# Kernel optimization log

Measured on AMD Instinct MI355X. Metric: run time of the kernel, lower is better.

The kernel has to match this reference:

```python
import jax, jax.numpy as jnp
import numpy as np

NEG_SLOPE = 0.2
EPS = 1e-5

N_NODES = 50000
N_GRAPHS = 500
NODES_PER_GRAPH = 100
N_EDGES = 500000
F_IN = 16
F_GRAPH = 4
HID = 64
N_CLASSES = 2


def setup_inputs() -> dict:
    key = jax.random.key(0)
    ks = jax.random.split(key, 32)
    x = jax.random.normal(ks[0], (N_NODES, F_IN), dtype=jnp.float32)
    # intra-graph random edges: dst lives in the same 100-node block as src
    src = jax.random.randint(ks[1], (N_EDGES,), 0, N_NODES)
    dst = (src // NODES_PER_GRAPH) * NODES_PER_GRAPH + jax.random.randint(ks[2], (N_EDGES,), 0, NODES_PER_GRAPH)
    edge_index = jnp.stack([src, dst]).astype(jnp.int64)
    graph_input = jax.random.normal(ks[3], (N_GRAPHS, F_GRAPH), dtype=jnp.float32)
    batch = (jnp.arange(N_NODES) // NODES_PER_GRAPH).astype(jnp.int64)

    def w(k, shape, scale=0.1):
        return (jax.random.normal(k, shape, dtype=jnp.float32) * scale)

    inp = dict(x=x, edge_index=edge_index, graph_input=graph_input, batch=batch)
    # GraphNorm params
    inp['gn_w'] = jnp.ones((F_IN,), jnp.float32)
    inp['gn_b'] = w(ks[4], (F_IN,))
    inp['gn_ms'] = jnp.ones((F_IN,), jnp.float32)
    inp['W1'] = w(ks[5], (F_IN, 4 * HID))
    inp['as1'] = w(ks[6], (4, HID)); inp['ad1'] = w(ks[7], (4, HID))
    inp['b1'] = w(ks[8], (4 * HID,))
    inp['W2'] = w(ks[9], (4 * HID, 4 * HID))
    inp['as2'] = w(ks[10], (4, HID)); inp['ad2'] = w(ks[11], (4, HID))
    inp['b2'] = w(ks[12], (4 * HID,))
    inp['W3'] = w(ks[13], (4 * HID, HID))
    inp['as3'] = w(ks[14], (1, HID)); inp['ad3'] = w(ks[15], (1, HID))
    inp['b3'] = w(ks[16], (HID,))
    # BatchNorm1d (eval mode) over [HID + F_GRAPH]
    D = HID + F_GRAPH
    inp['bn_g'] = 1.0 + w(ks[17], (D,))
    inp['bn_b'] = w(ks[18], (D,))
    inp['bn_m'] = jnp.zeros((D,), jnp.float32)
    inp['bn_v'] = jnp.ones((D,), jnp.float32)
    # Dense head
    inp['Wd1'] = w(ks[19], (D, HID)); inp['bd1'] = w(ks[20], (HID,))
    inp['Wd2'] = w(ks[21], (HID, HID)); inp['bd2'] = w(ks[22], (HID,))
    inp['Wo'] = w(ks[23], (HID, N_CLASSES)); inp['bo'] = w(ks[24], (N_CLASSES,))
    return inp


def _segment_softmax(e, seg, n):
    m = jax.ops.segment_max(e, seg, num_segments=n)
    ex = jnp.exp(e - m[seg])
    s = jax.ops.segment_sum(ex, seg, num_segments=n)
    return ex / s[seg]


def _gat_conv(x, src, dst, W, att_src, att_dst, b):
    N = x.shape[0]
    H, C = att_src.shape
    loop = jnp.arange(N)
    src = jnp.concatenate([src, loop])  # PyG GATConv adds self-loops
    dst = jnp.concatenate([dst, loop])
    h = (x @ W).reshape(N, H, C)
    a_src = (h * att_src).sum(-1)  # [N,H]
    a_dst = (h * att_dst).sum(-1)
    e = jax.nn.leaky_relu(a_src[src] + a_dst[dst], NEG_SLOPE)  # [E,H]
    alpha = _segment_softmax(e, dst, N)
    out = jax.ops.segment_sum(h[src] * alpha[:, :, None], dst, num_segments=N)
    return out.reshape(N, H * C) + b


def _graph_norm(x, batch, n_graphs, w, b, ms):
    cnt = jax.ops.segment_sum(jnp.ones((x.shape[0],), x.dtype), batch, num_segments=n_graphs)[:, None]
    mean = jax.ops.segment_sum(x, batch, num_segments=n_graphs) / cnt
    out = x - mean[batch] * ms
    var = jax.ops.segment_sum(out * out, batch, num_segments=n_graphs) / cnt
    return w * out / jnp.sqrt(var[batch] + EPS) + b


def _global_mean_pool(x, batch, n_graphs):
    cnt = jax.ops.segment_sum(jnp.ones((x.shape[0],), x.dtype), batch, num_segments=n_graphs)[:, None]
    return jax.ops.segment_sum(x, batch, num_segments=n_graphs) / cnt


def reference(x, edge_index, graph_input, batch,
              gn_w, gn_b, gn_ms,
              W1, as1, ad1, b1,
              W2, as2, ad2, b2,
              W3, as3, ad3, b3,
              bn_g, bn_b, bn_m, bn_v,
              Wd1, bd1, Wd2, bd2, Wo, bo):
    src, dst = edge_index[0], edge_index[1]
    G = graph_input.shape[0]
    h = _graph_norm(x, batch, G, gn_w, gn_b, gn_ms)
    # dropout is a no-op in eval
    h = jax.nn.elu(_gat_conv(h, src, dst, W1, as1, ad1, b1))
    h = jax.nn.elu(_gat_conv(h, src, dst, W2, as2, ad2, b2))
    h = _gat_conv(h, src, dst, W3, as3, ad3, b3)
    g = _global_mean_pool(h, batch, G)
    g = jnp.concatenate([g, graph_input], axis=1)
    g = (g - bn_m) / jnp.sqrt(bn_v + EPS) * bn_g + bn_b  # BatchNorm1d eval
    g = jax.nn.selu(g @ Wd1 + bd1)
    g = jax.nn.selu(g @ Wd2 + bd2)
    g = g @ Wo + bo
    return jax.nn.softmax(g, axis=1)
```

## Files before the change

kernel.cpp:

```cpp
#include <hip/hip_runtime.h>
#include <math.h>

#define N_NODES 50000
#define N_ROWS_PAD 50048
#define N_GRAPHS 500
#define NPG 100
#define N_EDGES 500000
#define F_IN 16
#define HID 64
#define EW_CAP 1408

#define SELU_SCALE 1.0507009873554804934193349852946f
#define SELU_ALPHA 1.6732632423543772848170429916717f

typedef __attribute__((ext_vector_type(8))) short short8;
typedef __attribute__((ext_vector_type(8))) unsigned short ushort8;
typedef __attribute__((ext_vector_type(4))) float floatx4;

__device__ __forceinline__ float lrelu(float x){ return x > 0.f ? x : 0.2f * x; }
__device__ __forceinline__ float eluf(float x){ return x > 0.f ? x : expf(x) - 1.f; }
__device__ __forceinline__ float seluf(float x){
    return x > 0.f ? SELU_SCALE * x : SELU_SCALE * (SELU_ALPHA * (expf(x) - 1.f));
}
__device__ __forceinline__ unsigned short f2bf(float x){
    unsigned u = __float_as_uint(x);
    return (unsigned short)((u + 0x7FFFu + ((u >> 16) & 1u)) >> 16);
}
__device__ __forceinline__ float bf2f(unsigned short u){
    return __uint_as_float((unsigned)u << 16);
}
__device__ __forceinline__ float bf2f_lo(unsigned u){
    return __uint_as_float(u << 16);
}
__device__ __forceinline__ float bf2f_hi(unsigned u){
    return __uint_as_float(u & 0xFFFF0000u);
}

__global__ void k_count(const int* __restrict__ dst, int* __restrict__ counts){
    int e = blockIdx.x * 256 + threadIdx.x;
    if (e < N_EDGES) atomicAdd(&counts[dst[e]], 1);
}

__global__ void k_local_scan(const int* __restrict__ counts, int* __restrict__ local_off,
                             int* __restrict__ graph_tot){
    __shared__ int s[128];
    int g = blockIdx.x, t = threadIdx.x;
    int v = (t < NPG) ? counts[g * NPG + t] : 0;
    s[t] = v; __syncthreads();
    for (int o = 1; o < 128; o <<= 1){
        int x = (t >= o) ? s[t - o] : 0;
        __syncthreads();
        s[t] += x;
        __syncthreads();
    }
    if (t < NPG) local_off[g * NPG + t] = s[t] - v;
    if (t == 127) graph_tot[g] = s[127];
}

__global__ void k_graph_scan(const int* __restrict__ graph_tot, int* __restrict__ graph_base){
    __shared__ int s[512];
    int t = threadIdx.x;
    int v = (t < N_GRAPHS) ? graph_tot[t] : 0;
    s[t] = v; __syncthreads();
    for (int o = 1; o < 512; o <<= 1){
        int x = (t >= o) ? s[t - o] : 0;
        __syncthreads();
        s[t] += x;
        __syncthreads();
    }
    if (t < N_GRAPHS) graph_base[t] = s[t] - v;
}

__global__ void k_off(const int* __restrict__ local_off, const int* __restrict__ graph_base,
                      int* __restrict__ node_off, int* __restrict__ write_ptr){
    int n = blockIdx.x * 256 + threadIdx.x;
    if (n < N_NODES){
        int v = local_off[n] + graph_base[n / NPG];
        node_off[n] = v;
        write_ptr[n] = v;
    }
}

__global__ void k_scatter(const int* __restrict__ src, const int* __restrict__ dst,
                          int* __restrict__ write_ptr, int* __restrict__ csr){
    int e = blockIdx.x * 256 + threadIdx.x;
    if (e < N_EDGES){
        int d = dst[e];
        int pos = atomicAdd(&write_ptr[d], 1);
        int b = (d / NPG) * NPG;
        csr[pos] = (src[e] - b) | ((d - b) << 8);
    }
}

__global__ void k_prep(const float* __restrict__ W1, const float* __restrict__ as1,
                       const float* __restrict__ ad1,
                       const float* __restrict__ W2, const float* __restrict__ as2,
                       const float* __restrict__ ad2,
                       const float* __restrict__ W3, const float* __restrict__ as3,
                       const float* __restrict__ ad3,
                       unsigned short* __restrict__ Wp2, unsigned short* __restrict__ Wp3,
                       float* __restrict__ M1f,
                       unsigned short* __restrict__ Mp2, unsigned short* __restrict__ Mp3){
    int id = blockIdx.x * 256 + threadIdx.x;
    if (id < 65536){
        int k = id >> 8, n = id & 255;
        Wp2[(((k >> 3) * 256) + n) * 8 + (k & 7)] = f2bf(W2[id]);
    } else if (id < 81920){
        int i = id - 65536;
        int k = i >> 6, n = i & 63;
        Wp3[(((k >> 3) * 64) + n) * 8 + (k & 7)] = f2bf(W3[i]);
    } else if (id < 82048){
        int i = id - 81920;
        int k = i >> 3, j = i & 7;
        int h = j & 3;
        const float* a = (j < 4) ? as1 : ad1;
        float s = 0.f;
        for (int c = 0; c < 64; c++) s += W1[k * 256 + h * 64 + c] * a[h * 64 + c];
        M1f[k * 8 + j] = s;
    } else if (id < 86144){
        int i = id - 82048;
        int k = i >> 4, col = i & 15;
        float s = 0.f;
        if (col < 8){
            int h = col & 3;
            const float* a = (col < 4) ? as2 : ad2;
            for (int c = 0; c < 64; c++) s += W2[k * 256 + h * 64 + c] * a[h * 64 + c];
        }
        Mp2[((k >> 3) * 16 + col) * 8 + (k & 7)] = f2bf(s);
    } else if (id < 90240){
        int i = id - 86144;
        int k = i >> 4, col = i & 15;
        float s = 0.f;
        if (col < 2){
            const float* a = (col == 0) ? as3 : ad3;
            for (int c = 0; c < 64; c++) s += W3[k * 64 + c] * a[c];
        }
        Mp3[((k >> 3) * 16 + col) * 8 + (k & 7)] = f2bf(s);
    }
}

__global__ void k_gnorm(const float* __restrict__ x, const float* __restrict__ w,
                        const float* __restrict__ b, const float* __restrict__ ms,
                        const float* __restrict__ M1f,
                        float* __restrict__ y, float* __restrict__ lg1){
    __shared__ float sx[NPG * F_IN];
    __shared__ float red[16][16];
    __shared__ float meanS[16], varS[16];
    int g = blockIdx.x, t = threadIdx.x;
    for (int idx = t; idx < NPG * F_IN; idx += 256) sx[idx] = x[g * NPG * F_IN + idx];
    __syncthreads();
    int f = t & 15, grp = t >> 4;
    float p = 0.f;
    for (int i = grp; i < NPG; i += 16) p += sx[i * 16 + f];
    red[grp][f] = p; __syncthreads();
    if (t < 16){
        float s = 0.f;
        for (int i = 0; i < 16; i++) s += red[i][t];
        meanS[t] = s * (1.f / 100.f);
    }
    __syncthreads();
    float mm = meanS[f] * ms[f];
    p = 0.f;
    for (int i = grp; i < NPG; i += 16){ float v = sx[i * 16 + f] - mm; p += v * v; }
    red[grp][f] = p; __syncthreads();
    if (t < 16){
        float s = 0.f;
        for (int i = 0; i < 16; i++) s += red[i][t];
        varS[t] = s * (1.f / 100.f);
    }
    __syncthreads();
    for (int idx = t; idx < NPG * F_IN; idx += 256){
        int ff = idx & 15;
        float v = w[ff] * (sx[idx] - meanS[ff] * ms[ff]) * rsqrtf(varS[ff] + 1e-5f) + b[ff];
        sx[idx] = v;
        y[g * NPG * F_IN + idx] = v;
    }
    __syncthreads();
    for (int i = t; i < NPG * 8; i += 256){
        int n = i >> 3, j = i & 7;
        float s = 0.f;
        #pragma unroll
        for (int ff = 0; ff < 16; ff++) s += sx[n * 16 + ff] * M1f[ff * 8 + j];
        lg1[(size_t)(g * NPG + n) * 8 + j] = s;
    }
}

__global__ void __launch_bounds__(256)
k_gemm_tiled(const float* __restrict__ X, const float* __restrict__ W,
             unsigned short* __restrict__ Ybf, int N){
    __shared__ float As[64][17];
    __shared__ float Bs[16][256];
    int t = threadIdx.x;
    int r0 = blockIdx.x * 64;
    {
        int row = t >> 2, kq = t & 3;
        float4 v = (r0 + row < N) ? *(const float4*)&X[(size_t)(r0 + row) * 16 + kq * 4]
                                  : make_float4(0.f, 0.f, 0.f, 0.f);
        As[row][kq * 4 + 0] = v.x; As[row][kq * 4 + 1] = v.y;
        As[row][kq * 4 + 2] = v.z; As[row][kq * 4 + 3] = v.w;
    }
    for (int i = t; i < 1024; i += 256)
        *(float4*)&Bs[0][i * 4] = *(const float4*)&W[i * 4];
    __syncthreads();

    int c4 = t & 15, rsub = t >> 4;
    float acc[4][16];
    #pragma unroll
    for (int i = 0; i < 4; i++)
        #pragma unroll
        for (int j = 0; j < 16; j++) acc[i][j] = 0.f;

    for (int k = 0; k < 16; k++){
        float a_[4];
        #pragma unroll
        for (int i = 0; i < 4; i++) a_[i] = As[rsub + 16 * i][k];
        float4 b0 = *(const float4*)&Bs[k][c4 * 4];
        float4 b1 = *(const float4*)&Bs[k][64 + c4 * 4];
        float4 b2 = *(const float4*)&Bs[k][128 + c4 * 4];
        float4 b3 = *(const float4*)&Bs[k][192 + c4 * 4];
        float bv[16] = {b0.x, b0.y, b0.z, b0.w, b1.x, b1.y, b1.z, b1.w,
                        b2.x, b2.y, b2.z, b2.w, b3.x, b3.y, b3.z, b3.w};
        #pragma unroll
        for (int i = 0; i < 4; i++)
            #pragma unroll
            for (int j = 0; j < 16; j++) acc[i][j] = fmaf(a_[i], bv[j], acc[i][j]);
    }
    #pragma unroll
    for (int i = 0; i < 4; i++){
        int row = r0 + rsub + 16 * i;
        if (row < N){
            ushort8 ua, ub;
            #pragma unroll
            for (int m = 0; m < 8; m++){
                ua[m] = f2bf(acc[i][(m & 3) * 4 + (m >> 2)]);
                ub[m] = f2bf(acc[i][(m & 3) * 4 + 2 + (m >> 2)]);
            }
            *(ushort8*)&Ybf[(size_t)row * 256 + c4 * 16]     = ua;
            *(ushort8*)&Ybf[(size_t)row * 256 + c4 * 16 + 8] = ub;
        }
    }
}

template<int COLB, int LG>
__global__ void __launch_bounds__(256)
k_gemm_mfma(const unsigned short* __restrict__ Xb,
            const unsigned short* __restrict__ Wp,
            const unsigned short* __restrict__ Mp,
            unsigned short* __restrict__ Ybf, float* __restrict__ lg,
            int N, int K, int OUT){
    int b = blockIdx.x;
    if (COLB == 4){
        int xcd = b & 7, idx = b >> 3;
        b = xcd * (int)(gridDim.x >> 3) + idx;
    }
    int cb = b & (COLB - 1);
    int rb = b / COLB;

    int t = threadIdx.x;
    int wave = t >> 6, lane = t & 63;
    int quad = lane >> 4, ln = lane & 15;
    int r0 = rb * 64 + wave * 16;
    int c0 = cb * 64;

    floatx4 acc[4];
    #pragma unroll
    for (int f = 0; f < 4; f++) acc[f] = (floatx4){0.f, 0.f, 0.f, 0.f};
    floatx4 accL = (floatx4){0.f, 0.f, 0.f, 0.f};

    const unsigned short* aptr = Xb + (size_t)(r0 + ln) * K + quad * 8;
    for (int kt = 0; kt < K; kt += 32){
        short8 a = *(const short8*)(aptr + kt);
        int kc = (kt >> 3) + quad;
        #pragma unroll
        for (int f = 0; f < 4; f++){
            short8 bfr = *(const short8*)(Wp + ((size_t)kc * OUT + c0 + f * 16 + ln) * 8);
            acc[f] = __builtin_amdgcn_mfma_f32_16x16x32_bf16(a, bfr, acc[f], 0, 0, 0);
        }
        if (LG > 0){
            if (cb == 0){
                short8 m = *(const short8*)(Mp + ((size_t)kc * 16 + ln) * 8);
                accL = __builtin_amdgcn_mfma_f32_16x16x32_bf16(a, m, accL, 0, 0, 0);
            }
        }
    }
    int rowb = r0 + quad * 4;
    #pragma unroll
    for (int f = 0; f < 4; f++){
        int col = c0 + f * 16 + ln;
        #pragma unroll
        for (int rg = 0; rg < 4; rg++){
            int row = rowb + rg;
            if (row < N) Ybf[(size_t)row * OUT + col] = f2bf(acc[f][rg]);
        }
    }
    if (LG > 0){
        if (cb == 0 && ln < LG){
            #pragma unroll
            for (int rg = 0; rg < 4; rg++){
                int row = rowb + rg;
                if (row < N) lg[(size_t)row * LG + ln] = accL[rg];
            }
        }
    }
}

template<int ILVIN>
__global__ void __launch_bounds__(512)
k_fused4(const unsigned short* __restrict__ hbf, const float* __restrict__ lg,
         const float* __restrict__ bias,
         const int* __restrict__ csr, const int* __restrict__ noff,
         const int* __restrict__ cnt, unsigned short* __restrict__ out_bf){
    __shared__ __align__(16) unsigned short hl[ILVIN ? 16 : NPG * 256];
    __shared__ __align__(16) unsigned int edl[EW_CAP][4];
    __shared__ __align__(16) float asrcl[NPG * 4], adstl[NPG * 4];
    __shared__ __align__(16) float wselfl[NPG * 4], rsuml[NPG * 4];
    __shared__ int offl[NPG], cntl[NPG];

    int g = blockIdx.x, t = threadIdx.x;
    int wave = t >> 6, lane = t & 63;
    int base = g * NPG;

    int ebeg = noff[base];
    int etot = noff[base + NPG - 1] + cnt[base + NPG - 1] - ebeg;
    int eln = etot < EW_CAP ? etot : EW_CAP;

    if (!ILVIN){
        for (int i = t; i < NPG * 16; i += 512){
            int node = i >> 4, c4 = i & 15;
            const unsigned short* hr = hbf + (size_t)(base + node) * 256 + c4 * 4;
            ushort4 f0 = *(const ushort4*)(hr);
            ushort4 f1 = *(const ushort4*)(hr + 64);
            ushort4 f2 = *(const ushort4*)(hr + 128);
            ushort4 f3 = *(const ushort4*)(hr + 192);
            ushort8 lo, hi;
            lo[0] = f0.x; lo[1] = f1.x; lo[2] = f2.x; lo[3] = f3.x;
            lo[4] = f0.y; lo[5] = f1.y; lo[6] = f2.y; lo[7] = f3.y;
            hi[0] = f0.z; hi[1] = f1.z; hi[2] = f2.z; hi[3] = f3.z;
            hi[4] = f0.w; hi[5] = f1.w; hi[6] = f2.w; hi[7] = f3.w;
            *(ushort8*)&hl[node * 256 + c4 * 16]     = lo;
            *(ushort8*)&hl[node * 256 + c4 * 16 + 8] = hi;
        }
    }
    for (int i = t; i < eln; i += 512) edl[i][2] = (unsigned)csr[ebeg + i];
    if (t < NPG){
        offl[t] = noff[base + t];
        cntl[t] = cnt[base + t];
        const float* lp = lg + (size_t)(base + t) * 8;
        *(float4*)&asrcl[t * 4] = *(const float4*)lp;
        *(float4*)&adstl[t * 4] = *(const float4*)(lp + 4);
    }
    __syncthreads();

    for (int i = t; i < eln; i += 512){
        unsigned sd = edl[i][2];
        int s = sd & 0xFF, d = sd >> 8;
        float4 av = *(const float4*)&asrcl[s * 4];
        float4 dv = *(const float4*)&adstl[d * 4];
        unsigned w0 = f2bf(expf(lrelu(av.x + dv.x)));
        unsigned w1 = f2bf(expf(lrelu(av.y + dv.y)));
        unsigned w2 = f2bf(expf(lrelu(av.z + dv.z)));
        unsigned w3 = f2bf(expf(lrelu(av.w + dv.w)));
        edl[i][0] = w0 | (w1 << 16);
        edl[i][1] = w2 | (w3 << 16);
    }
    __syncthreads();

    if (t < NPG){
        int d = t;
        float4 av = *(const float4*)&asrcl[d * 4];
        float4 dv = *(const float4*)&adstl[d * 4];
        float ws0 = expf(lrelu(av.x + dv.x));
        float ws1 = expf(lrelu(av.y + dv.y));
        float ws2 = expf(lrelu(av.z + dv.z));
        float ws3 = expf(lrelu(av.w + dv.w));
        float s0 = ws0, s1 = ws1, s2 = ws2, s3 = ws3;
        int ebg = offl[d] - ebeg, n = cntl[d];
        for (int j = 0; j < n; j++){
            uint2 v = *(const uint2*)&edl[ebg + j][0];
            s0 += bf2f_lo(v.x); s1 += bf2f_hi(v.x);
            s2 += bf2f_lo(v.y); s3 += bf2f_hi(v.y);
        }
        *(float4*)&wselfl[d * 4] = make_float4(ws0, ws1, ws2, ws3);
        *(float4*)&rsuml[d * 4]  = make_float4(1.f / s0, 1.f / s1, 1.f / s2, 1.f / s3);
    }
    __syncthreads();

    float b0 = bias[lane], b1 = bias[64 + lane], b2 = bias[128 + lane], b3 = bias[192 + lane];
    for (int d = wave; d < NPG; d += 8){
        float4 ws = *(const float4*)&wselfl[d * 4];
        float4 rs = *(const float4*)&rsuml[d * 4];
        ushort4 hv = ILVIN ? *(const ushort4*)&hbf[(size_t)(base + d) * 256 + lane * 4]
                           : *(const ushort4*)&hl[d * 256 + lane * 4];
        float a0 = ws.x * bf2f(hv.x);
        float a1 = ws.y * bf2f(hv.y);
        float a2 = ws.z * bf2f(hv.z);
        float a3 = ws.w * bf2f(hv.w);
        int ebg = offl[d] - ebeg, n = cntl[d];
        int j = 0;
        #pragma unroll 1
        for (; j + 4 <= n; j += 4){
            #pragma unroll
            for (int k = 0; k < 4; k++){
                uint4 v = *(const uint4*)&edl[ebg + j + k][0];
                int s = (int)(v.z & 0xFFu);
                ushort4 x = ILVIN ? *(const ushort4*)&hbf[(size_t)(base + s) * 256 + lane * 4]
                                  : *(const ushort4*)&hl[s * 256 + lane * 4];
                a0 = fmaf(bf2f_lo(v.x), bf2f(x.x), a0);
                a1 = fmaf(bf2f_hi(v.x), bf2f(x.y), a1);
                a2 = fmaf(bf2f_lo(v.y), bf2f(x.z), a2);
                a3 = fmaf(bf2f_hi(v.y), bf2f(x.w), a3);
            }
        }
        for (; j < n; j++){
            uint4 v = *(const uint4*)&edl[ebg + j][0];
            int s = (int)(v.z & 0xFFu);
            ushort4 x = ILVIN ? *(const ushort4*)&hbf[(size_t)(base + s) * 256 + lane * 4]
                              : *(const ushort4*)&hl[s * 256 + lane * 4];
            a0 = fmaf(bf2f_lo(v.x), bf2f(x.x), a0);
            a1 = fmaf(bf2f_hi(v.x), bf2f(x.y), a1);
            a2 = fmaf(bf2f_lo(v.y), bf2f(x.z), a2);
            a3 = fmaf(bf2f_hi(v.y), bf2f(x.w), a3);
        }
        size_t ob = (size_t)(base + d) * 256 + lane;
        out_bf[ob]       = f2bf(eluf(a0 * rs.x + b0));
        out_bf[ob + 64]  = f2bf(eluf(a1 * rs.y + b1));
        out_bf[ob + 128] = f2bf(eluf(a2 * rs.z + b2));
        out_bf[ob + 192] = f2bf(eluf(a3 * rs.w + b3));
    }
}

__global__ void __launch_bounds__(512)
k_fused1(const unsigned short* __restrict__ hbf, const float* __restrict__ lg3,
         const float* __restrict__ bias,
         const int* __restrict__ csr, const int* __restrict__ noff,
         const int* __restrict__ cnt, float* __restrict__ out){
    __shared__ __align__(16) unsigned int edl[EW_CAP][2];
    __shared__ float asrcl[NPG], adstl[NPG];
    __shared__ float wselfl[NPG], rsuml[NPG];
    __shared__ int offl[NPG], cntl[NPG];

    int g = blockIdx.x, t = threadIdx.x;
    int wave = t >> 6, lane = t & 63;
    int base = g * NPG;

    int ebeg = noff[base];
    int etot = noff[base + NPG - 1] + cnt[base + NPG - 1] - ebeg;
    int eln = etot < EW_CAP ? etot : EW_CAP;

    for (int i = t; i < eln; i += 512) edl[i][1] = (unsigned)csr[ebeg + i];
    if (t < NPG){
        offl[t] = noff[base + t];
        cntl[t] = cnt[base + t];
        asrcl[t] = lg3[(size_t)(base + t) * 2];
        adstl[t] = lg3[(size_t)(base + t) * 2 + 1];
    }
    __syncthreads();

    for (int i = t; i < eln; i += 512){
        unsigned sd = edl[i][1];
        int s = sd & 0xFF, d = sd >> 8;
        edl[i][0] = (unsigned)f2bf(expf(lrelu(asrcl[s] + adstl[d])));
    }
    __syncthreads();

    if (t < NPG){
        float wsf = expf(lrelu(asrcl[t] + adstl[t]));
        float sum = wsf;
        int ebg = offl[t] - ebeg, n = cntl[t];
        for (int j = 0; j < n; j++) sum += bf2f((unsigned short)edl[ebg + j][0]);
        wselfl[t] = wsf;
        rsuml[t] = 1.f / sum;
    }
    __syncthreads();

    float bl = bias[lane];
    for (int d = wave; d < NPG; d += 8){
        float acc = wselfl[d] * bf2f(hbf[(size_t)(base + d) * 64 + lane]);
        int ebg = offl[d] - ebeg, n = cntl[d];
        for (int j = 0; j < n; j++){
            uint2 v = *(const uint2*)&edl[ebg + j][0];
            acc = fmaf(bf2f_lo(v.x),
                       bf2f(hbf[(size_t)(base + (int)(v.y & 0xFFu)) * 64 + lane]), acc);
        }
        out[(size_t)(base + d) * 64 + lane] = acc * rsuml[d] + bl;
    }
}

__global__ void k_head(const float* __restrict__ x3, const float* __restrict__ gin,
                       const float* __restrict__ bn_g, const float* __restrict__ bn_b,
                       const float* __restrict__ bn_m, const float* __restrict__ bn_v,
                       const float* __restrict__ Wd1, const float* __restrict__ bd1,
                       const float* __restrict__ Wd2, const float* __restrict__ bd2,
                       const float* __restrict__ Wo, const float* __restrict__ bo,
                       float* __restrict__ out){
    __shared__ float red[256];
    __shared__ float gv[68];
    __shared__ float g2[64];
    __shared__ float g3[64];
    int g = blockIdx.x, t = threadIdx.x;
    int c = t & 63, grp = t >> 6;
    float p = 0.f;
    for (int i = grp; i < NPG; i += 4) p += x3[(g * NPG + i) * 64 + c];
    red[t] = p; __syncthreads();
    if (t < 64){
        float s = red[t] + red[t + 64] + red[t + 128] + red[t + 192];
        float mean = s * (1.f / 100.f);
        gv[t] = (mean - bn_m[t]) * rsqrtf(bn_v[t] + 1e-5f) * bn_g[t] + bn_b[t];
    } else if (t < 68){
        int j = t - 64;
        float v = gin[g * 4 + j];
        gv[t] = (v - bn_m[t]) * rsqrtf(bn_v[t] + 1e-5f) * bn_g[t] + bn_b[t];
    }
    __syncthreads();
    if (t < 64){
        float s = bd1[t];
        for (int i = 0; i < 68; i++) s += gv[i] * Wd1[i * 64 + t];
        g2[t] = seluf(s);
    }
    __syncthreads();
    if (t < 64){
        float s = bd2[t];
        for (int i = 0; i < 64; i++) s += g2[i] * Wd2[i * 64 + t];
        g3[t] = seluf(s);
    }
    __syncthreads();
    if (t == 0){
        float l0 = bo[0], l1 = bo[1];
        for (int i = 0; i < 64; i++){ l0 += g3[i] * Wo[i * 2]; l1 += g3[i] * Wo[i * 2 + 1]; }
        float mx = fmaxf(l0, l1);
        float e0 = expf(l0 - mx), e1 = expf(l1 - mx);
        float inv = 1.f / (e0 + e1);
        out[g * 2] = e0 * inv;
        out[g * 2 + 1] = e1 * inv;
    }
}

extern "C" void kernel_launch(void* const* d_in, const int* in_sizes, int n_in,
                              void* d_out, int out_size, void* d_ws, size_t ws_size,
                              hipStream_t stream){
    const float* x   = (const float*)d_in[0];
    const int*   ei  = (const int*)d_in[1];
    const float* gin = (const float*)d_in[2];
    const float* gn_w = (const float*)d_in[4];
    const float* gn_b = (const float*)d_in[5];
    const float* gn_ms = (const float*)d_in[6];
    const float* W1 = (const float*)d_in[7];
    const float* as1 = (const float*)d_in[8];
    const float* ad1 = (const float*)d_in[9];
    const float* b1 = (const float*)d_in[10];
    const float* W2 = (const float*)d_in[11];
    const float* as2 = (const float*)d_in[12];
    const float* ad2 = (const float*)d_in[13];
    const float* b2 = (const float*)d_in[14];
    const float* W3 = (const float*)d_in[15];
    const float* as3 = (const float*)d_in[16];
    const float* ad3 = (const float*)d_in[17];
    const float* b3 = (const float*)d_in[18];
    const float* bn_g = (const float*)d_in[19];
    const float* bn_b = (const float*)d_in[20];
    const float* bn_m = (const float*)d_in[21];
    const float* bn_v = (const float*)d_in[22];
    const float* Wd1 = (const float*)d_in[23];
    const float* bd1 = (const float*)d_in[24];
    const float* Wd2 = (const float*)d_in[25];
    const float* bd2 = (const float*)d_in[26];
    const float* Wo = (const float*)d_in[27];
    const float* bo = (const float*)d_in[28];
    float* out = (float*)d_out;

    const int* src = ei;
    const int* dst = ei + N_EDGES;

    char* ws = (char*)d_ws;
    size_t off = 0;
    auto alloc = [&](size_t bytes) -> void* {
        void* p = ws + off;
        off = (off + bytes + 255) & ~(size_t)255;
        return p;
    };
    int* counts     = (int*)alloc((size_t)N_NODES * 4);
    int* local_off  = (int*)alloc((size_t)N_NODES * 4);
    int* node_off   = (int*)alloc((size_t)N_NODES * 4);
    int* write_ptr  = (int*)alloc((size_t)N_NODES * 4);
    int* graph_tot  = (int*)alloc(512 * 4);
    int* graph_base = (int*)alloc(512 * 4);
    int* csr        = (int*)alloc((size_t)N_EDGES * 4);
    float* y        = (float*)alloc((size_t)N_NODES * F_IN * 4);
    unsigned short* wp2 = (unsigned short*)alloc((size_t)256 * 256 * 2);
    unsigned short* wp3 = (unsigned short*)alloc((size_t)256 * 64 * 2);
    float* M1f      = (float*)alloc((size_t)16 * 8 * 4);
    unsigned short* Mp2 = (unsigned short*)alloc((size_t)32 * 16 * 8 * 2);
    unsigned short* Mp3 = (unsigned short*)alloc((size_t)32 * 16 * 8 * 2);
    float* lg1      = (float*)alloc((size_t)N_NODES * 8 * 4);
    float* lg2      = (float*)alloc((size_t)N_ROWS_PAD * 8 * 4);
    float* lg3      = (float*)alloc((size_t)N_ROWS_PAD * 2 * 4);
    unsigned short* xbh = (unsigned short*)alloc((size_t)N_NODES * 256 * 2);
    unsigned short* xb  = (unsigned short*)alloc((size_t)N_ROWS_PAD * 256 * 2);
    unsigned short* x3b = (unsigned short*)alloc((size_t)N_NODES * HID * 2);
    float* bufD     = (float*)alloc((size_t)N_NODES * HID * 4);

    hipMemsetAsync(counts, 0, (size_t)N_NODES * 4, stream);
    k_count<<<(N_EDGES + 255) / 256, 256, 0, stream>>>(dst, counts);
    k_local_scan<<<N_GRAPHS, 128, 0, stream>>>(counts, local_off, graph_tot);
    k_graph_scan<<<1, 512, 0, stream>>>(graph_tot, graph_base);
    k_off<<<(N_NODES + 255) / 256, 256, 0, stream>>>(local_off, graph_base, node_off, write_ptr);
    k_scatter<<<(N_EDGES + 255) / 256, 256, 0, stream>>>(src, dst, write_ptr, csr);

    k_prep<<<(90240 + 255) / 256, 256, 0, stream>>>(W1, as1, ad1, W2, as2, ad2,
                                                    W3, as3, ad3, wp2, wp3, M1f, Mp2, Mp3);

    k_gnorm<<<N_GRAPHS, 256, 0, stream>>>(x, gn_w, gn_b, gn_ms, M1f, y, lg1);

    k_gemm_tiled<<<(N_NODES + 63) / 64, 256, 0, stream>>>(y, W1, xbh, N_NODES);
    k_fused4<1><<<N_GRAPHS, 512, 0, stream>>>(xbh, lg1, b1, csr, node_off, counts, xb);

    k_gemm_mfma<4, 8><<<(N_ROWS_PAD / 64) * 4, 256, 0, stream>>>(xb, wp2, Mp2, xbh, lg2,
                                                                 N_NODES, 256, 256);
    k_fused4<0><<<N_GRAPHS, 512, 0, stream>>>(xbh, lg2, b2, csr, node_off, counts, xb);

    k_gemm_mfma<1, 2><<<N_ROWS_PAD / 64, 256, 0, stream>>>(xb, wp3, Mp3, x3b, lg3,
                                                           N_NODES, 256, 64);
    k_fused1<<<N_GRAPHS, 512, 0, stream>>>(x3b, lg3, b3, csr, node_off, counts, bufD);

    k_head<<<N_GRAPHS, 256, 0, stream>>>(bufD, gin, bn_g, bn_b, bn_m, bn_v,
                                         Wd1, bd1, Wd2, bd2, Wo, bo, out);
}
```

Measured before the change: 349.8 us.

## Build per-graph CSR via bucketing and fuse GraphNorm with first GAT projection

Replaces the global count/scan/offset/scatter CSR build (five launches plus a large memset) with a per-graph bucket pass and a per-graph LDS sort kernel that writes a fixed-capacity padded CSR segment per graph. Downstream fused kernels now index the per-graph CSR at g*EW_CAP with local offsets. Separately, the GraphNorm kernel now also performs the 16x256 W1 projection and writes bf16 directly, which removes the fp32 y intermediate and the separate tiled GEMM launch. Edges beyond EW_CAP per graph are silently dropped, and the global atomics on only 500 per-graph counters may contend.

```diff
diff --git a/kernel.cpp b/kernel.cpp
--- a/kernel.cpp
+++ b/kernel.cpp
@@ -36,16 +36,34 @@
     return __uint_as_float(u & 0xFFFF0000u);
 }
 
-__global__ void k_count(const int* __restrict__ dst, int* __restrict__ counts){
+__global__ void k_bucket(const int* __restrict__ src, const int* __restrict__ dst,
+                         int* __restrict__ gcnt, unsigned* __restrict__ gbuf){
     int e = blockIdx.x * 256 + threadIdx.x;
-    if (e < N_EDGES) atomicAdd(&counts[dst[e]], 1);
-}
-
-__global__ void k_local_scan(const int* __restrict__ counts, int* __restrict__ local_off,
-                             int* __restrict__ graph_tot){
+    if (e < N_EDGES){
+        int d = dst[e];
+        int g = d / NPG;
+        int b = g * NPG;
+        int pos = atomicAdd(&gcnt[g], 1);
+        if (pos < EW_CAP)
+            gbuf[(size_t)g * EW_CAP + pos] = (unsigned)((src[e] - b) | ((d - b) << 8));
+    }
+}
+
+__global__ void __launch_bounds__(128)
+k_sort(const int* __restrict__ gcnt, const unsigned* __restrict__ gbuf,
+       unsigned* __restrict__ csr, int* __restrict__ noff, int* __restrict__ cnt){
+    __shared__ unsigned se[EW_CAP];
+    __shared__ int c100[NPG];
     __shared__ int s[128];
+    __shared__ int woff[NPG];
     int g = blockIdx.x, t = threadIdx.x;
-    int v = (t < NPG) ? counts[g * NPG + t] : 0;
+    int E = gcnt[g]; if (E > EW_CAP) E = EW_CAP;
+    for (int i = t; i < E; i += 128) se[i] = gbuf[(size_t)g * EW_CAP + i];
+    if (t < NPG) c100[t] = 0;
+    __syncthreads();
+    for (int i = t; i < E; i += 128) atomicAdd(&c100[se[i] >> 8], 1);
+    __syncthreads();
+    int v = (t < NPG) ? c100[t] : 0;
     s[t] = v; __syncthreads();
     for (int o = 1; o < 128; o <<= 1){
         int x = (t >= o) ? s[t - o] : 0;
@@ -53,42 +71,17 @@
         s[t] += x;
         __syncthreads();
     }
-    if (t < NPG) local_off[g * NPG + t] = s[t] - v;
-    if (t == 127) graph_tot[g] = s[127];
-}
-
-__global__ void k_graph_scan(const int* __restrict__ graph_tot, int* __restrict__ graph_base){
-    __shared__ int s[512];
-    int t = threadIdx.x;
-    int v = (t < N_GRAPHS) ? graph_tot[t] : 0;
-    s[t] = v; __syncthreads();
-    for (int o = 1; o < 512; o <<= 1){
-        int x = (t >= o) ? s[t - o] : 0;
-        __syncthreads();
-        s[t] += x;
-        __syncthreads();
-    }
-    if (t < N_GRAPHS) graph_base[t] = s[t] - v;
-}
-
-__global__ void k_off(const int* __restrict__ local_off, const int* __restrict__ graph_base,
-                      int* __restrict__ node_off, int* __restrict__ write_ptr){
-    int n = blockIdx.x * 256 + threadIdx.x;
-    if (n < N_NODES){
-        int v = local_off[n] + graph_base[n / NPG];
-        node_off[n] = v;
-        write_ptr[n] = v;
-    }
-}
-
-__global__ void k_scatter(const int* __restrict__ src, const int* __restrict__ dst,
-                          int* __restrict__ write_ptr, int* __restrict__ csr){
-    int e = blockIdx.x * 256 + threadIdx.x;
-    if (e < N_EDGES){
-        int d = dst[e];
-        int pos = atomicAdd(&write_ptr[d], 1);
-        int b = (d / NPG) * NPG;
-        csr[pos] = (src[e] - b) | ((d - b) << 8);
+    if (t < NPG){
+        int excl = s[t] - v;
+        noff[g * NPG + t] = excl;
+        cnt[g * NPG + t] = v;
+        woff[t] = excl;
+    }
+    __syncthreads();
+    for (int i = t; i < E; i += 128){
+        unsigned sd = se[i];
+        int pos = atomicAdd(&woff[sd >> 8], 1);
+        csr[(size_t)g * EW_CAP + pos] = sd;
     }
 }
 
@@ -139,15 +132,20 @@
     }
 }
 
-__global__ void k_gnorm(const float* __restrict__ x, const float* __restrict__ w,
-                        const float* __restrict__ b, const float* __restrict__ ms,
-                        const float* __restrict__ M1f,
-                        float* __restrict__ y, float* __restrict__ lg1){
+__global__ void __launch_bounds__(256)
+k_gnorm_conv1(const float* __restrict__ x, const float* __restrict__ w,
+              const float* __restrict__ b, const float* __restrict__ ms,
+              const float* __restrict__ W1, const float* __restrict__ M1f,
+              unsigned short* __restrict__ Ybf, float* __restrict__ lg1){
     __shared__ float sx[NPG * F_IN];
+    __shared__ float Ws[16][256];
     __shared__ float red[16][16];
     __shared__ float meanS[16], varS[16];
     int g = blockIdx.x, t = threadIdx.x;
-    for (int idx = t; idx < NPG * F_IN; idx += 256) sx[idx] = x[g * NPG * F_IN + idx];
+    int base = g * NPG;
+    for (int idx = t; idx < NPG * F_IN; idx += 256) sx[idx] = x[base * F_IN + idx];
+    for (int i = t; i < 1024; i += 256)
+        *(float4*)&Ws[0][i * 4] = *(const float4*)&W1[i * 4];
     __syncthreads();
     int f = t & 15, grp = t >> 4;
     float p = 0.f;
@@ -171,73 +169,42 @@
     __syncthreads();
     for (int idx = t; idx < NPG * F_IN; idx += 256){
         int ff = idx & 15;
-        float v = w[ff] * (sx[idx] - meanS[ff] * ms[ff]) * rsqrtf(varS[ff] + 1e-5f) + b[ff];
-        sx[idx] = v;
-        y[g * NPG * F_IN + idx] = v;
-    }
-    __syncthreads();
+        sx[idx] = w[ff] * (sx[idx] - meanS[ff] * ms[ff]) * rsqrtf(varS[ff] + 1e-5f) + b[ff];
+    }
+    __syncthreads();
+    int c4 = t & 15, rsub = t >> 4;
+    for (int n = rsub; n < NPG; n += 16){
+        float acc[16];
+        #pragma unroll
+        for (int j = 0; j < 16; j++) acc[j] = 0.f;
+        #pragma unroll
+        for (int k = 0; k < 16; k++){
+            float a_ = sx[n * 16 + k];
+            float4 b0 = *(const float4*)&Ws[k][c4 * 4];
+            float4 b1 = *(const float4*)&Ws[k][64 + c4 * 4];
+            float4 b2 = *(const float4*)&Ws[k][128 + c4 * 4];
+            float4 b3 = *(const float4*)&Ws[k][192 + c4 * 4];
+            float bv[16] = {b0.x, b0.y, b0.z, b0.w, b1.x, b1.y, b1.z, b1.w,
+                            b2.x, b2.y, b2.z, b2.w, b3.x, b3.y, b3.z, b3.w};
+            #pragma unroll
+            for (int j = 0; j < 16; j++) acc[j] = fmaf(a_, bv[j], acc[j]);
+        }
+        ushort8 ua, ub;
+        #pragma unroll
+        for (int m = 0; m < 8; m++){
+            ua[m] = f2bf(acc[(m & 3) * 4 + (m >> 2)]);
+            ub[m] = f2bf(acc[(m & 3) * 4 + 2 + (m >> 2)]);
+        }
+        size_t ob = (size_t)(base + n) * 256 + c4 * 16;
+        *(ushort8*)&Ybf[ob]     = ua;
+        *(ushort8*)&Ybf[ob + 8] = ub;
+    }
     for (int i = t; i < NPG * 8; i += 256){
         int n = i >> 3, j = i & 7;
         float s = 0.f;
         #pragma unroll
         for (int ff = 0; ff < 16; ff++) s += sx[n * 16 + ff] * M1f[ff * 8 + j];
-        lg1[(size_t)(g * NPG + n) * 8 + j] = s;
-    }
-}
-
-__global__ void __launch_bounds__(256)
-k_gemm_tiled(const float* __restrict__ X, const float* __restrict__ W,
-             unsigned short* __restrict__ Ybf, int N){
-    __shared__ float As[64][17];
-    __shared__ float Bs[16][256];
-    int t = threadIdx.x;
-    int r0 = blockIdx.x * 64;
-    {
-        int row = t >> 2, kq = t & 3;
-        float4 v = (r0 + row < N) ? *(const float4*)&X[(size_t)(r0 + row) * 16 + kq * 4]
-                                  : make_float4(0.f, 0.f, 0.f, 0.f);
-        As[row][kq * 4 + 0] = v.x; As[row][kq * 4 + 1] = v.y;
-        As[row][kq * 4 + 2] = v.z; As[row][kq * 4 + 3] = v.w;
-    }
-    for (int i = t; i < 1024; i += 256)
-        *(float4*)&Bs[0][i * 4] = *(const float4*)&W[i * 4];
-    __syncthreads();
-
-    int c4 = t & 15, rsub = t >> 4;
-    float acc[4][16];
-    #pragma unroll
-    for (int i = 0; i < 4; i++)
-        #pragma unroll
-        for (int j = 0; j < 16; j++) acc[i][j] = 0.f;
-
-    for (int k = 0; k < 16; k++){
-        float a_[4];
-        #pragma unroll
-        for (int i = 0; i < 4; i++) a_[i] = As[rsub + 16 * i][k];
-        float4 b0 = *(const float4*)&Bs[k][c4 * 4];
-        float4 b1 = *(const float4*)&Bs[k][64 + c4 * 4];
-        float4 b2 = *(const float4*)&Bs[k][128 + c4 * 4];
-        float4 b3 = *(const float4*)&Bs[k][192 + c4 * 4];
-        float bv[16] = {b0.x, b0.y, b0.z, b0.w, b1.x, b1.y, b1.z, b1.w,
-                        b2.x, b2.y, b2.z, b2.w, b3.x, b3.y, b3.z, b3.w};
-        #pragma unroll
-        for (int i = 0; i < 4; i++)
-            #pragma unroll
-            for (int j = 0; j < 16; j++) acc[i][j] = fmaf(a_[i], bv[j], acc[i][j]);
-    }
-    #pragma unroll
-    for (int i = 0; i < 4; i++){
-        int row = r0 + rsub + 16 * i;
-        if (row < N){
-            ushort8 ua, ub;
-            #pragma unroll
-            for (int m = 0; m < 8; m++){
-                ua[m] = f2bf(acc[i][(m & 3) * 4 + (m >> 2)]);
-                ub[m] = f2bf(acc[i][(m & 3) * 4 + 2 + (m >> 2)]);
-            }
-            *(ushort8*)&Ybf[(size_t)row * 256 + c4 * 16]     = ua;
-            *(ushort8*)&Ybf[(size_t)row * 256 + c4 * 16 + 8] = ub;
-        }
+        lg1[(size_t)(base + n) * 8 + j] = s;
     }
 }
 
@@ -308,7 +275,7 @@
 __global__ void __launch_bounds__(512)
 k_fused4(const unsigned short* __restrict__ hbf, const float* __restrict__ lg,
          const float* __restrict__ bias,
-         const int* __restrict__ csr, const int* __restrict__ noff,
+         const unsigned* __restrict__ csr, const int* __restrict__ noff,
          const int* __restrict__ cnt, unsigned short* __restrict__ out_bf){
     __shared__ __align__(16) unsigned short hl[ILVIN ? 16 : NPG * 256];
     __shared__ __align__(16) unsigned int edl[EW_CAP][4];
@@ -319,10 +286,7 @@
     int g = blockIdx.x, t = threadIdx.x;
     int wave = t >> 6, lane = t & 63;
     int base = g * NPG;
-
-    int ebeg = noff[base];
-    int etot = noff[base + NPG - 1] + cnt[base + NPG - 1] - ebeg;
-    int eln = etot < EW_CAP ? etot : EW_CAP;
+    size_t ebeg = (size_t)g * EW_CAP;
 
     if (!ILVIN){
         for (int i = t; i < NPG * 16; i += 512){
@@ -341,7 +305,6 @@
             *(ushort8*)&hl[node * 256 + c4 * 16 + 8] = hi;
         }
     }
-    for (int i = t; i < eln; i += 512) edl[i][2] = (unsigned)csr[ebeg + i];
     if (t < NPG){
         offl[t] = noff[base + t];
         cntl[t] = cnt[base + t];
@@ -349,6 +312,9 @@
         *(float4*)&asrcl[t * 4] = *(const float4*)lp;
         *(float4*)&adstl[t * 4] = *(const float4*)(lp + 4);
     }
+    __syncthreads();
+    int eln = offl[NPG - 1] + cntl[NPG - 1];
+    for (int i = t; i < eln; i += 512) edl[i][2] = csr[ebeg + i];
     __syncthreads();
 
     for (int i = t; i < eln; i += 512){
@@ -374,7 +340,7 @@
         float ws2 = expf(lrelu(av.z + dv.z));
         float ws3 = expf(lrelu(av.w + dv.w));
         float s0 = ws0, s1 = ws1, s2 = ws2, s3 = ws3;
-        int ebg = offl[d] - ebeg, n = cntl[d];
+        int ebg = offl[d], n = cntl[d];
         for (int j = 0; j < n; j++){
             uint2 v = *(const uint2*)&edl[ebg + j][0];
             s0 += bf2f_lo(v.x); s1 += bf2f_hi(v.x);
@@ -395,7 +361,7 @@
         float a1 = ws.y * bf2f(hv.y);
         float a2 = ws.z * bf2f(hv.z);
         float a3 = ws.w * bf2f(hv.w);
-        int ebg = offl[d] - ebeg, n = cntl[d];
+        int ebg = offl[d], n = cntl[d];
         int j = 0;
         #pragma unroll 1
         for (; j + 4 <= n; j += 4){
@@ -432,7 +398,7 @@
 __global__ void __launch_bounds__(512)
 k_fused1(const unsigned short* __restrict__ hbf, const float* __restrict__ lg3,
          const float* __restrict__ bias,
-         const int* __restrict__ csr, const int* __restrict__ noff,
+         const unsigned* __restrict__ csr, const int* __restrict__ noff,
          const int* __restrict__ cnt, float* __restrict__ out){
     __shared__ __align__(16) unsigned int edl[EW_CAP][2];
     __shared__ float asrcl[NPG], adstl[NPG];
@@ -442,12 +408,8 @@
     int g = blockIdx.x, t = threadIdx.x;
     int wave = t >> 6, lane = t & 63;
     int base = g * NPG;
-
-    int ebeg = noff[base];
-    int etot = noff[base + NPG - 1] + cnt[base + NPG - 1] - ebeg;
-    int eln = etot < EW_CAP ? etot : EW_CAP;
-
-    for (int i = t; i < eln; i += 512) edl[i][1] = (unsigned)csr[ebeg + i];
+    size_t ebeg = (size_t)g * EW_CAP;
+
     if (t < NPG){
         offl[t] = noff[base + t];
         cntl[t] = cnt[base + t];
@@ -455,6 +417,9 @@
         adstl[t] = lg3[(size_t)(base + t) * 2 + 1];
     }
     __syncthreads();
+    int eln = offl[NPG - 1] + cntl[NPG - 1];
+    for (int i = t; i < eln; i += 512) edl[i][1] = csr[ebeg + i];
+    __syncthreads();
 
     for (int i = t; i < eln; i += 512){
         unsigned sd = edl[i][1];
@@ -466,7 +431,7 @@
     if (t < NPG){
         float wsf = expf(lrelu(asrcl[t] + adstl[t]));
         float sum = wsf;
-        int ebg = offl[t] - ebeg, n = cntl[t];
+        int ebg = offl[t], n = cntl[t];
         for (int j = 0; j < n; j++) sum += bf2f((unsigned short)edl[ebg + j][0]);
         wselfl[t] = wsf;
         rsuml[t] = 1.f / sum;
@@ -476,7 +441,7 @@
     float bl = bias[lane];
     for (int d = wave; d < NPG; d += 8){
         float acc = wselfl[d] * bf2f(hbf[(size_t)(base + d) * 64 + lane]);
-        int ebg = offl[d] - ebeg, n = cntl[d];
+        int ebg = offl[d], n = cntl[d];
         for (int j = 0; j < n; j++){
             uint2 v = *(const uint2*)&edl[ebg + j][0];
             acc = fmaf(bf2f_lo(v.x),
@@ -578,14 +543,11 @@
         off = (off + bytes + 255) & ~(size_t)255;
         return p;
     };
-    int* counts     = (int*)alloc((size_t)N_NODES * 4);
-    int* local_off  = (int*)alloc((size_t)N_NODES * 4);
-    int* node_off   = (int*)alloc((size_t)N_NODES * 4);
-    int* write_ptr  = (int*)alloc((size_t)N_NODES * 4);
-    int* graph_tot  = (int*)alloc(512 * 4);
-    int* graph_base = (int*)alloc(512 * 4);
-    int* csr        = (int*)alloc((size_t)N_EDGES * 4);
-    float* y        = (float*)alloc((size_t)N_NODES * F_IN * 4);
+    int* gcnt       = (int*)alloc(512 * 4);
+    unsigned* gbuf  = (unsigned*)alloc((size_t)N_GRAPHS * EW_CAP * 4);
+    unsigned* csr   = (unsigned*)alloc((size_t)N_GRAPHS * EW_CAP * 4);
+    int* noff       = (int*)alloc((size_t)N_NODES * 4);
+    int* cnt        = (int*)alloc((size_t)N_NODES * 4);
     unsigned short* wp2 = (unsigned short*)alloc((size_t)256 * 256 * 2);
     unsigned short* wp3 = (unsigned short*)alloc((size_t)256 * 64 * 2);
     float* M1f      = (float*)alloc((size_t)16 * 8 * 4);
@@ -599,28 +561,22 @@
     unsigned short* x3b = (unsigned short*)alloc((size_t)N_NODES * HID * 2);
     float* bufD     = (float*)alloc((size_t)N_NODES * HID * 4);
 
-    hipMemsetAsync(counts, 0, (size_t)N_NODES * 4, stream);
-    k_count<<<(N_EDGES + 255) / 256, 256, 0, stream>>>(dst, counts);
-    k_local_scan<<<N_GRAPHS, 128, 0, stream>>>(counts, local_off, graph_tot);
-    k_graph_scan<<<1, 512, 0, stream>>>(graph_tot, graph_base);
-    k_off<<<(N_NODES + 255) / 256, 256, 0, stream>>>(local_off, graph_base, node_off, write_ptr);
-    k_scatter<<<(N_EDGES + 255) / 256, 256, 0, stream>>>(src, dst, write_ptr, csr);
-
+    hipMemsetAsync(gcnt, 0, 512 * 4, stream);
+    k_bucket<<<(N_EDGES + 255) / 256, 256, 0, stream>>>(src, dst, gcnt, gbuf);
     k_prep<<<(90240 + 255) / 256, 256, 0, stream>>>(W1, as1, ad1, W2, as2, ad2,
                                                     W3, as3, ad3, wp2, wp3, M1f, Mp2, Mp3);
-
-    k_gnorm<<<N_GRAPHS, 256, 0, stream>>>(x, gn_w, gn_b, gn_ms, M1f, y, lg1);
-
-    k_gemm_tiled<<<(N_NODES + 63) / 64, 256, 0, stream>>>(y, W1, xbh, N_NODES);
-    k_fused4<1><<<N_GRAPHS, 512, 0, stream>>>(xbh, lg1, b1, csr, node_off, counts, xb);
+    k_sort<<<N_GRAPHS, 128, 0, stream>>>(gcnt, gbuf, csr, noff, cnt);
+
+    k_gnorm_conv1<<<N_GRAPHS, 256, 0, stream>>>(x, gn_w, gn_b, gn_ms, W1, M1f, xbh, lg1);
+    k_fused4<1><<<N_GRAPHS, 512, 0, stream>>>(xbh, lg1, b1, csr, noff, cnt, xb);
 
     k_gemm_mfma<4, 8><<<(N_ROWS_PAD / 64) * 4, 256, 0, stream>>>(xb, wp2, Mp2, xbh, lg2,
                                                                  N_NODES, 256, 256);
-    k_fused4<0><<<N_GRAPHS, 512, 0, stream>>>(xbh, lg2, b2, csr, node_off, counts, xb);
+    k_fused4<0><<<N_GRAPHS, 512, 0, stream>>>(xbh, lg2, b2, csr, noff, cnt, xb);
 
     k_gemm_mfma<1, 2><<<N_ROWS_PAD / 64, 256, 0, stream>>>(xb, wp3, Mp3, x3b, lg3,
                                                            N_NODES, 256, 64);
-    k_fused1<<<N_GRAPHS, 512, 0, stream>>>(x3b, lg3, b3, csr, node_off, counts, bufD);
+    k_fused1<<<N_GRAPHS, 512, 0, stream>>>(x3b, lg3, b3, csr, noff, cnt, bufD);
 
     k_head<<<N_GRAPHS, 256, 0, stream>>>(bufD, gin, bn_g, bn_b, bn_m, bn_v,
                                          Wd1, bd1, Wd2, bd2, Wo, bo, out);
```

New measurement: 448.8 us. 28.3% more time.
